# Kernel tuning notes

Measured on AMD Instinct MI355X. Metric: run time of the kernel, lower is better.

Reference implementation:

```python
import jax, jax.numpy as jnp
import numpy as np

DIM = 192
HEADS = 6
HEAD_DIM = DIM // HEADS  # 32
N = 64                   # prod(window_size) = 4*4*4
BW = 4096                # num_windows * B
NEG = -1e9               # finite stand-in for -inf additive mask


def setup_inputs() -> dict:
    key = jax.random.key(0)
    k_x, k_m, k_qkv, k_p, k_pb = jax.random.split(key, 5)
    x = jax.random.normal(k_x, (BW, N, N and 192))  # (BW, N, C)
    x = jax.random.normal(k_x, (BW, N, DIM), dtype=jnp.float32)
    # Shifted-window style additive mask: block-diagonal groups of tokens.
    # Each window gets a random group id per token; tokens attend only within
    # their group (0), cross-group gets NEG. Diagonal always allowed.
    gid = jax.random.randint(k_m, (BW, N), 0, 3)  # (BW, N) group ids in {0,1,2}
    same = gid[:, :, None] == gid[:, None, :]     # (BW, N, N) bool
    mask = jnp.where(same, 0.0, NEG).astype(jnp.float32)[:, None, :, :]  # (BW,1,N,N)
    w_qkv = jax.random.normal(k_qkv, (3 * DIM, DIM), dtype=jnp.float32) * (DIM ** -0.5)
    w_proj = jax.random.normal(k_p, (DIM, DIM), dtype=jnp.float32) * (DIM ** -0.5)
    b_proj = jax.random.normal(k_pb, (DIM,), dtype=jnp.float32) * 0.02
    return {"x": x, "mask": mask, "w_qkv": w_qkv, "w_proj": w_proj, "b_proj": b_proj}


def reference(x, mask, w_qkv, w_proj, b_proj):
    b, n, c = x.shape
    scale = HEAD_DIM ** -0.5
    # qkv linear (no bias) then split: 'b n (three heads c) -> three b heads n c'
    qkv = jnp.einsum('bnc,dc->bnd', x, w_qkv)               # (b, n, 3*C)
    qkv = qkv.reshape(b, n, 3, HEADS, HEAD_DIM)
    qkv = jnp.transpose(qkv, (2, 0, 3, 1, 4))               # (3, b, heads, n, hd)
    q, k, v = qkv[0], qkv[1], qkv[2]
    q = q * scale
    # scaled_dot_product_attention with additive mask (scale=1 since q pre-scaled)
    scores = jnp.einsum('bhqd,bhkd->bhqk', q, k) + mask     # (b, heads, n, n)
    probs = jax.nn.softmax(scores, axis=-1)
    out = jnp.einsum('bhqk,bhkd->bhqd', probs, v)           # (b, heads, n, hd)
    # 'b k n c -> b n (k c)'
    out = jnp.transpose(out, (0, 2, 1, 3)).reshape(b, n, c)
    # output projection (bias=True in nn.Linear default)
    return jnp.einsum('bnc,dc->bnd', out, w_proj) + b_proj
```

## Files before the change

kernel.cpp:

```cpp
#include <hip/hip_runtime.h>

#define NTOK 64
#define DIM 192
#define HD 32

#define RS  200
#define VTS 68
#define WQN (576 * DIM)
#define WPN (DIM * DIM)

typedef __attribute__((ext_vector_type(8))) short short8;
typedef __attribute__((ext_vector_type(4))) float floatx4;
typedef __attribute__((ext_vector_type(2))) unsigned int uint2v;

__device__ __forceinline__ short f2bf(float f) {
    union { float f; unsigned int u; } c; c.f = f;
    unsigned int r = (c.u + 0x7FFFu + ((c.u >> 16) & 1u)) >> 16;
    return (short)(unsigned short)r;
}

__device__ __forceinline__ unsigned pkbf(float a, float b) {
    unsigned ua = __float_as_uint(a); ua += 0x7FFFu + ((ua >> 16) & 1u);
    unsigned ub = __float_as_uint(b); ub += 0x7FFFu + ((ub >> 16) & 1u);
    return __builtin_amdgcn_perm(ub, ua, 0x07060302u);
}

__device__ __forceinline__ short8 cvt8(const float* p) {
    const float4* v = reinterpret_cast<const float4*>(p);
    float4 lo = v[0], hi = v[1];
    union { unsigned u[4]; short8 s; } r;
    r.u[0] = pkbf(lo.x, lo.y);
    r.u[1] = pkbf(lo.z, lo.w);
    r.u[2] = pkbf(hi.x, hi.y);
    r.u[3] = pkbf(hi.z, hi.w);
    return r.s;
}

__device__ __forceinline__ short8 qshuf(floatx4 v0, floatx4 v1, int lane) {
    const int q = lane >> 4;
    const unsigned p0a = pkbf(v0[0], v0[1]);
    const unsigned p0b = pkbf(v0[2], v0[3]);
    const unsigned p1a = pkbf(v1[0], v1[1]);
    const unsigned p1b = pkbf(v1[2], v1[3]);
    const int s0 = (lane & 15) | ((q & 1) << 5);
    const int s1 = s0 + 16;
    const unsigned l0 = (unsigned)__shfl((int)p0a, s0);
    const unsigned h0 = (unsigned)__shfl((int)p1a, s0);
    const unsigned l1 = (unsigned)__shfl((int)p0b, s0);
    const unsigned h1 = (unsigned)__shfl((int)p1b, s0);
    const unsigned l2 = (unsigned)__shfl((int)p0a, s1);
    const unsigned h2 = (unsigned)__shfl((int)p1a, s1);
    const unsigned l3 = (unsigned)__shfl((int)p0b, s1);
    const unsigned h3 = (unsigned)__shfl((int)p1b, s1);
    const bool hi = q >= 2;
    union { unsigned u[4]; short8 s; } ret;
    ret.u[0] = hi ? h0 : l0;
    ret.u[1] = hi ? h1 : l1;
    ret.u[2] = hi ? h2 : l2;
    ret.u[3] = hi ? h3 : l3;
    return ret.s;
}

__global__ void wprep(const float* __restrict__ wqkv, const float* __restrict__ wproj,
                      short* __restrict__ wqb, short* __restrict__ wpb) {
    const int i = blockIdx.x * 256 + (int)threadIdx.x;
    for (int e = i; e < WQN; e += 192 * 256) {
        float v = wqkv[e];
        if (e < DIM * DIM) v *= 0.17677669529663688f;
        wqb[e] = f2bf(v);
    }
    for (int e = i; e < WPN; e += 192 * 256) wpb[e] = f2bf(wproj[e]);
}

template <int WS>
__global__ __launch_bounds__(256, 2)
void wattn_fused(const float* __restrict__ x, const float* __restrict__ mask,
                 const float* __restrict__ wqkv, const float* __restrict__ wproj,
                 const float* __restrict__ bproj, float* __restrict__ out,
                 const short* __restrict__ wqb, const short* __restrict__ wpb) {
    __shared__ short ksm[NTOK * RS];
    __shared__ short vsT[DIM * VTS];
    __shared__ short osm[NTOK * RS];

    const int bw   = blockIdx.x;
    const int tid  = (int)threadIdx.x;
    const int wave = tid >> 6;
    const int lane = tid & 63;
    const int r    = lane & 15;
    const int q    = lane >> 4;

    const float* xb = x + (size_t)bw * (NTOK * DIM);

    auto ldq = [&](int off) -> short8 {
        if constexpr (WS) return *reinterpret_cast<const short8*>(wqb + off);
        else              return cvt8(wqkv + off);
    };
    auto ldp = [&](int off) -> short8 {
        if constexpr (WS) return *reinterpret_cast<const short8*>(wpb + off);
        else              return cvt8(wproj + off);
    };

    {
        short8 a[4][6];
        #pragma unroll
        for (int mt = 0; mt < 4; ++mt) {
            #pragma unroll
            for (int s = 0; s < 6; ++s)
                a[mt][s] = cvt8(xb + (mt * 16 + r) * DIM + s * 32 + q * 8);
        }

        if (wave < 2) {
            #pragma unroll 1
            for (int nt = 0; nt < 6; ++nt) {
                const int dk = wave * 96 + nt * 16;
                floatx4 acc[4];
                #pragma unroll
                for (int mt = 0; mt < 4; ++mt) acc[mt] = (floatx4){0.f, 0.f, 0.f, 0.f};
                #pragma unroll
                for (int s = 0; s < 6; ++s) {
                    const short8 b8 = ldq((DIM + dk + r) * DIM + s * 32 + q * 8);
                    #pragma unroll
                    for (int mt = 0; mt < 4; ++mt)
                        acc[mt] = __builtin_amdgcn_mfma_f32_16x16x32_bf16(b8, a[mt][s], acc[mt], 0, 0, 0);
                }
                #pragma unroll
                for (int mt = 0; mt < 4; ++mt) {
                    uint2v u;
                    u.x = pkbf(acc[mt][0], acc[mt][1]);
                    u.y = pkbf(acc[mt][2], acc[mt][3]);
                    *reinterpret_cast<uint2v*>(ksm + (mt * 16 + r) * RS + dk + q * 4) = u;
                }
            }
        } else {
            #pragma unroll 1
            for (int nt = 0; nt < 6; ++nt) {
                const int dv = (wave - 2) * 96 + nt * 16;
                floatx4 acc[4];
                #pragma unroll
                for (int mt = 0; mt < 4; ++mt) acc[mt] = (floatx4){0.f, 0.f, 0.f, 0.f};
                #pragma unroll
                for (int s = 0; s < 6; ++s) {
                    const short8 b8 = ldq((2 * DIM + dv + r) * DIM + s * 32 + q * 8);
                    #pragma unroll
                    for (int mt = 0; mt < 4; ++mt)
                        acc[mt] = __builtin_amdgcn_mfma_f32_16x16x32_bf16(a[mt][s], b8, acc[mt], 0, 0, 0);
                }
                #pragma unroll
                for (int mt = 0; mt < 4; ++mt) {
                    uint2v u;
                    u.x = pkbf(acc[mt][0], acc[mt][1]);
                    u.y = pkbf(acc[mt][2], acc[mt][3]);
                    *reinterpret_cast<uint2v*>(vsT + (dv + r) * VTS + mt * 16 + q * 4) = u;
                }
            }
        }
    }
    __builtin_amdgcn_sched_barrier(0);
    __syncthreads();

    const float* mb  = mask + (size_t)bw * (NTOK * NTOK);
    const float* mbl = mb + 256 * q + r;

    #pragma unroll 1
    for (int i = 0; i < 3; ++i) {
        const int uu = wave * 3 + i, h = uu >> 1, half = uu & 1;

        float mv[2][4][4];
        #pragma unroll
        for (int qt = 0; qt < 2; ++qt)
            #pragma unroll
            for (int kt = 0; kt < 4; ++kt)
                #pragma unroll
                for (int g = 0; g < 4; ++g)
                    mv[qt][kt][g] = mbl[kt * 1024 + g * 64 + half * 32 + qt * 16];

        floatx4 qa[2][2];
        #pragma unroll
        for (int dt = 0; dt < 2; ++dt)
            #pragma unroll
            for (int qt = 0; qt < 2; ++qt) qa[dt][qt] = (floatx4){0.f, 0.f, 0.f, 0.f};
        #pragma unroll
        for (int s = 0; s < 6; ++s) {
            const short8 w0 = ldq((h * HD + r) * DIM + s * 32 + q * 8);
            const short8 w1 = ldq((h * HD + 16 + r) * DIM + s * 32 + q * 8);
            #pragma unroll
            for (int qt = 0; qt < 2; ++qt) {
                const short8 xf = cvt8(xb + ((half * 2 + qt) * 16 + r) * DIM + s * 32 + q * 8);
                qa[0][qt] = __builtin_amdgcn_mfma_f32_16x16x32_bf16(w0, xf, qa[0][qt], 0, 0, 0);
                qa[1][qt] = __builtin_amdgcn_mfma_f32_16x16x32_bf16(w1, xf, qa[1][qt], 0, 0, 0);
            }
        }
        if constexpr (!WS) {
            #pragma unroll
            for (int dt = 0; dt < 2; ++dt)
                #pragma unroll
                for (int qt = 0; qt < 2; ++qt)
                    #pragma unroll
                    for (int g = 0; g < 4; ++g)
                        qa[dt][qt][g] *= 0.17677669529663688f;
        }
        short8 bq0 = qshuf(qa[0][0], qa[1][0], lane);
        short8 bq1 = qshuf(qa[0][1], qa[1][1], lane);

        short8 bk[4];
        #pragma unroll
        for (int kt = 0; kt < 4; ++kt)
            bk[kt] = *reinterpret_cast<const short8*>(ksm + (kt * 16 + r) * RS + h * HD + q * 8);

        floatx4 sa[4][2];
        #pragma unroll
        for (int kt = 0; kt < 4; ++kt) {
            floatx4 z = (floatx4){0.f, 0.f, 0.f, 0.f};
            sa[kt][0] = __builtin_amdgcn_mfma_f32_16x16x32_bf16(bk[kt], bq0, z, 0, 0, 0);
            sa[kt][1] = __builtin_amdgcn_mfma_f32_16x16x32_bf16(bk[kt], bq1, z, 0, 0, 0);
        }
        #pragma unroll
        for (int kt = 0; kt < 4; ++kt)
            #pragma unroll
            for (int qt = 0; qt < 2; ++qt)
                #pragma unroll
                for (int g = 0; g < 4; ++g)
                    sa[kt][qt][g] += mv[qt][kt][g];

        float rinv[2];
        #pragma unroll
        for (int qt = 0; qt < 2; ++qt) {
            float mx = sa[0][qt][0];
            #pragma unroll
            for (int kt = 0; kt < 4; ++kt)
                #pragma unroll
                for (int g = 0; g < 4; ++g) mx = fmaxf(mx, sa[kt][qt][g]);
            mx = fmaxf(mx, __shfl_xor(mx, 16));
            mx = fmaxf(mx, __shfl_xor(mx, 32));
            float sm = 0.f;
            #pragma unroll
            for (int kt = 0; kt < 4; ++kt) {
                #pragma unroll
                for (int g = 0; g < 4; ++g) {
                    float p = __expf(sa[kt][qt][g] - mx);
                    sa[kt][qt][g] = p;
                    sm += p;
                }
            }
            sm += __shfl_xor(sm, 16);
            sm += __shfl_xor(sm, 32);
            rinv[qt] = 1.0f / sm;
        }

        short8 ap[2][2];
        #pragma unroll
        for (int qt = 0; qt < 2; ++qt) {
            #pragma unroll
            for (int kk = 0; kk < 2; ++kk)
                ap[qt][kk] = qshuf(sa[2 * kk][qt], sa[2 * kk + 1][qt], lane);
        }

        short8 bv[2][2];
        #pragma unroll
        for (int nv = 0; nv < 2; ++nv)
            #pragma unroll
            for (int kk = 0; kk < 2; ++kk)
                bv[nv][kk] = *reinterpret_cast<const short8*>(
                    vsT + (h * HD + nv * 16 + r) * VTS + kk * 32 + q * 8);

        #pragma unroll
        for (int qt = 0; qt < 2; ++qt) {
            #pragma unroll
            for (int nv = 0; nv < 2; ++nv) {
                floatx4 o = (floatx4){0.f, 0.f, 0.f, 0.f};
                o = __builtin_amdgcn_mfma_f32_16x16x32_bf16(bv[nv][0], ap[qt][0], o, 0, 0, 0);
                o = __builtin_amdgcn_mfma_f32_16x16x32_bf16(bv[nv][1], ap[qt][1], o, 0, 0, 0);
                uint2v u;
                u.x = pkbf(o[0] * rinv[qt], o[1] * rinv[qt]);
                u.y = pkbf(o[2] * rinv[qt], o[3] * rinv[qt]);
                *reinterpret_cast<uint2v*>(
                    osm + (half * 32 + qt * 16 + r) * RS + h * HD + nv * 16 + q * 4) = u;
            }
        }
    }
    __syncthreads();

    short8 ao[4][6];
    #pragma unroll
    for (int mt = 0; mt < 4; ++mt) {
        #pragma unroll
        for (int s = 0; s < 6; ++s)
            ao[mt][s] = *reinterpret_cast<const short8*>(osm + (mt * 16 + r) * RS + s * 32 + q * 8);
    }

    float* ob = out + (size_t)bw * (NTOK * DIM);
    #pragma unroll 1
    for (int nt = 0; nt < 3; ++nt) {
        const int d0 = wave * 48 + nt * 16;
        const float4 b4 = *reinterpret_cast<const float4*>(bproj + d0 + q * 4);
        floatx4 acc[4];
        #pragma unroll
        for (int mt = 0; mt < 4; ++mt) acc[mt] = (floatx4){b4.x, b4.y, b4.z, b4.w};
        #pragma unroll
        for (int s = 0; s < 6; ++s) {
            const short8 w8 = ldp((d0 + r) * DIM + s * 32 + q * 8);
            #pragma unroll
            for (int mt = 0; mt < 4; ++mt)
                acc[mt] = __builtin_amdgcn_mfma_f32_16x16x32_bf16(w8, ao[mt][s], acc[mt], 0, 0, 0);
        }
        #pragma unroll
        for (int mt = 0; mt < 4; ++mt) {
            float4 st;
            st.x = acc[mt][0]; st.y = acc[mt][1]; st.z = acc[mt][2]; st.w = acc[mt][3];
            *reinterpret_cast<float4*>(ob + (mt * 16 + r) * DIM + d0 + q * 4) = st;
        }
    }
}

extern "C" void kernel_launch(void* const* d_in, const int* in_sizes, int n_in,
                              void* d_out, int out_size, void* d_ws, size_t ws_size,
                              hipStream_t stream) {
    const float* x    = (const float*)d_in[0];
    const float* mask = (const float*)d_in[1];
    const float* wqkv = (const float*)d_in[2];
    const float* wp   = (const float*)d_in[3];
    const float* bp   = (const float*)d_in[4];
    float* out = (float*)d_out;
    const int nblocks = in_sizes[0] / (NTOK * DIM);
    const size_t need = (size_t)(WQN + WPN) * sizeof(short);
    if (d_ws != nullptr && ws_size >= need) {
        short* wqb = (short*)d_ws;
        short* wpb = wqb + WQN;
        wprep<<<192, 256, 0, stream>>>(wqkv, wp, wqb, wpb);
        wattn_fused<1><<<nblocks, 256, 0, stream>>>(x, mask, wqkv, wp, bp, out, wqb, wpb);
    } else {
        wattn_fused<0><<<nblocks, 256, 0, stream>>>(x, mask, wqkv, wp, bp, out, nullptr, nullptr);
    }
}
```

Before: 700.7 us.

## Process eight windows per block with register-prefetched x and LDS-staged mask

Each block now loops over eight windows instead of one. The next window's x is prefetched into registers while the current one computes, and the mask is loaded coalesced and staged through shared memory instead of scattered per-lane loads. Q is computed from the already converted x registers rather than re-reading x from global memory. Launch bounds drop to one block per SM because of the larger register footprint and extra LDS, which lowers occupancy and cuts the grid to 512 blocks. Any window count not divisible by eight would be left unprocessed.

```diff
diff --git a/kernel.cpp b/kernel.cpp
--- a/kernel.cpp
+++ b/kernel.cpp
@@ -3,9 +3,11 @@
 #define NTOK 64
 #define DIM 192
 #define HD 32
+#define W 8
 
 #define RS  200
 #define VTS 68
+#define MS  68
 #define WQN (576 * DIM)
 #define WPN (DIM * DIM)
 
@@ -73,7 +75,7 @@
 }
 
 template <int WS>
-__global__ __launch_bounds__(256, 2)
+__global__ __launch_bounds__(256, 1)
 void wattn_fused(const float* __restrict__ x, const float* __restrict__ mask,
                  const float* __restrict__ wqkv, const float* __restrict__ wproj,
                  const float* __restrict__ bproj, float* __restrict__ out,
@@ -81,15 +83,14 @@
     __shared__ short ksm[NTOK * RS];
     __shared__ short vsT[DIM * VTS];
     __shared__ short osm[NTOK * RS];
-
-    const int bw   = blockIdx.x;
+    __shared__ float mlds[NTOK * MS];
+
+    const int bw0  = (int)blockIdx.x * W;
     const int tid  = (int)threadIdx.x;
     const int wave = tid >> 6;
     const int lane = tid & 63;
     const int r    = lane & 15;
     const int q    = lane >> 4;
-
-    const float* xb = x + (size_t)bw * (NTOK * DIM);
 
     auto ldq = [&](int off) -> short8 {
         if constexpr (WS) return *reinterpret_cast<const short8*>(wqb + off);
@@ -100,14 +101,46 @@
         else              return cvt8(wproj + off);
     };
 
-    {
+    float4 xp[4][6][2];
+    auto xload = [&](const float* xb) {
+        #pragma unroll
+        for (int mt = 0; mt < 4; ++mt) {
+            #pragma unroll
+            for (int s = 0; s < 6; ++s) {
+                const float4* v = reinterpret_cast<const float4*>(
+                    xb + (mt * 16 + r) * DIM + s * 32 + q * 8);
+                xp[mt][s][0] = v[0];
+                xp[mt][s][1] = v[1];
+            }
+        }
+    };
+    xload(x + (size_t)bw0 * (NTOK * DIM));
+
+    #pragma unroll 1
+    for (int w = 0; w < W; ++w) {
+        const int bw = bw0 + w;
+
         short8 a[4][6];
         #pragma unroll
         for (int mt = 0; mt < 4; ++mt) {
             #pragma unroll
-            for (int s = 0; s < 6; ++s)
-                a[mt][s] = cvt8(xb + (mt * 16 + r) * DIM + s * 32 + q * 8);
-        }
+            for (int s = 0; s < 6; ++s) {
+                union { unsigned u[4]; short8 s8; } t;
+                t.u[0] = pkbf(xp[mt][s][0].x, xp[mt][s][0].y);
+                t.u[1] = pkbf(xp[mt][s][0].z, xp[mt][s][0].w);
+                t.u[2] = pkbf(xp[mt][s][1].x, xp[mt][s][1].y);
+                t.u[3] = pkbf(xp[mt][s][1].z, xp[mt][s][1].w);
+                a[mt][s] = t.s8;
+            }
+        }
+
+        const float* mbW = mask + (size_t)bw * (NTOK * NTOK);
+        float4 mreg[4];
+        #pragma unroll
+        for (int it = 0; it < 4; ++it)
+            mreg[it] = *reinterpret_cast<const float4*>(mbW + it * 1024 + tid * 4);
+
+        if (w + 1 < W) xload(x + (size_t)(bw + 1) * (NTOK * DIM));
 
         if (wave < 2) {
             #pragma unroll 1
@@ -154,161 +187,151 @@
                 }
             }
         }
-    }
-    __builtin_amdgcn_sched_barrier(0);
-    __syncthreads();
-
-    const float* mb  = mask + (size_t)bw * (NTOK * NTOK);
-    const float* mbl = mb + 256 * q + r;
-
-    #pragma unroll 1
-    for (int i = 0; i < 3; ++i) {
-        const int uu = wave * 3 + i, h = uu >> 1, half = uu & 1;
-
-        float mv[2][4][4];
-        #pragma unroll
-        for (int qt = 0; qt < 2; ++qt)
+        #pragma unroll
+        for (int it = 0; it < 4; ++it)
+            *reinterpret_cast<float4*>(&mlds[(it * 16 + (tid >> 4)) * MS + (tid & 15) * 4]) = mreg[it];
+        __syncthreads();
+
+        #pragma unroll 1
+        for (int i = 0; i < 3; ++i) {
+            const int uu = wave * 3 + i, h = uu >> 1, half = uu & 1;
+
+            floatx4 qa[2][2];
+            #pragma unroll
+            for (int dt = 0; dt < 2; ++dt)
+                #pragma unroll
+                for (int qt = 0; qt < 2; ++qt) qa[dt][qt] = (floatx4){0.f, 0.f, 0.f, 0.f};
+            #pragma unroll
+            for (int s = 0; s < 6; ++s) {
+                const short8 w0 = ldq((h * HD + r) * DIM + s * 32 + q * 8);
+                const short8 w1 = ldq((h * HD + 16 + r) * DIM + s * 32 + q * 8);
+                #pragma unroll
+                for (int qt = 0; qt < 2; ++qt) {
+                    qa[0][qt] = __builtin_amdgcn_mfma_f32_16x16x32_bf16(w0, a[half * 2 + qt][s], qa[0][qt], 0, 0, 0);
+                    qa[1][qt] = __builtin_amdgcn_mfma_f32_16x16x32_bf16(w1, a[half * 2 + qt][s], qa[1][qt], 0, 0, 0);
+                }
+            }
+            if constexpr (!WS) {
+                #pragma unroll
+                for (int dt = 0; dt < 2; ++dt)
+                    #pragma unroll
+                    for (int qt = 0; qt < 2; ++qt)
+                        #pragma unroll
+                        for (int g = 0; g < 4; ++g)
+                            qa[dt][qt][g] *= 0.17677669529663688f;
+            }
+            short8 bq0 = qshuf(qa[0][0], qa[1][0], lane);
+            short8 bq1 = qshuf(qa[0][1], qa[1][1], lane);
+
+            short8 bk[4];
             #pragma unroll
             for (int kt = 0; kt < 4; ++kt)
-                #pragma unroll
-                for (int g = 0; g < 4; ++g)
-                    mv[qt][kt][g] = mbl[kt * 1024 + g * 64 + half * 32 + qt * 16];
-
-        floatx4 qa[2][2];
-        #pragma unroll
-        for (int dt = 0; dt < 2; ++dt)
-            #pragma unroll
-            for (int qt = 0; qt < 2; ++qt) qa[dt][qt] = (floatx4){0.f, 0.f, 0.f, 0.f};
-        #pragma unroll
-        for (int s = 0; s < 6; ++s) {
-            const short8 w0 = ldq((h * HD + r) * DIM + s * 32 + q * 8);
-            const short8 w1 = ldq((h * HD + 16 + r) * DIM + s * 32 + q * 8);
+                bk[kt] = *reinterpret_cast<const short8*>(ksm + (kt * 16 + r) * RS + h * HD + q * 8);
+
+            floatx4 sa[4][2];
+            #pragma unroll
+            for (int kt = 0; kt < 4; ++kt) {
+                floatx4 z = (floatx4){0.f, 0.f, 0.f, 0.f};
+                sa[kt][0] = __builtin_amdgcn_mfma_f32_16x16x32_bf16(bk[kt], bq0, z, 0, 0, 0);
+                sa[kt][1] = __builtin_amdgcn_mfma_f32_16x16x32_bf16(bk[kt], bq1, z, 0, 0, 0);
+            }
+            #pragma unroll
+            for (int kt = 0; kt < 4; ++kt)
+                #pragma unroll
+                for (int qt = 0; qt < 2; ++qt)
+                    #pragma unroll
+                    for (int g = 0; g < 4; ++g)
+                        sa[kt][qt][g] += mlds[(kt * 16 + 4 * q + g) * MS + half * 32 + qt * 16 + r];
+
+            float rinv[2];
             #pragma unroll
             for (int qt = 0; qt < 2; ++qt) {
-                const short8 xf = cvt8(xb + ((half * 2 + qt) * 16 + r) * DIM + s * 32 + q * 8);
-                qa[0][qt] = __builtin_amdgcn_mfma_f32_16x16x32_bf16(w0, xf, qa[0][qt], 0, 0, 0);
-                qa[1][qt] = __builtin_amdgcn_mfma_f32_16x16x32_bf16(w1, xf, qa[1][qt], 0, 0, 0);
-            }
-        }
-        if constexpr (!WS) {
-            #pragma unroll
-            for (int dt = 0; dt < 2; ++dt)
-                #pragma unroll
-                for (int qt = 0; qt < 2; ++qt)
-                    #pragma unroll
-                    for (int g = 0; g < 4; ++g)
-                        qa[dt][qt][g] *= 0.17677669529663688f;
-        }
-        short8 bq0 = qshuf(qa[0][0], qa[1][0], lane);
-        short8 bq1 = qshuf(qa[0][1], qa[1][1], lane);
-
-        short8 bk[4];
-        #pragma unroll
-        for (int kt = 0; kt < 4; ++kt)
-            bk[kt] = *reinterpret_cast<const short8*>(ksm + (kt * 16 + r) * RS + h * HD + q * 8);
-
-        floatx4 sa[4][2];
-        #pragma unroll
-        for (int kt = 0; kt < 4; ++kt) {
-            floatx4 z = (floatx4){0.f, 0.f, 0.f, 0.f};
-            sa[kt][0] = __builtin_amdgcn_mfma_f32_16x16x32_bf16(bk[kt], bq0, z, 0, 0, 0);
-            sa[kt][1] = __builtin_amdgcn_mfma_f32_16x16x32_bf16(bk[kt], bq1, z, 0, 0, 0);
-        }
-        #pragma unroll
-        for (int kt = 0; kt < 4; ++kt)
-            #pragma unroll
-            for (int qt = 0; qt < 2; ++qt)
-                #pragma unroll
-                for (int g = 0; g < 4; ++g)
-                    sa[kt][qt][g] += mv[qt][kt][g];
-
-        float rinv[2];
-        #pragma unroll
-        for (int qt = 0; qt < 2; ++qt) {
-            float mx = sa[0][qt][0];
-            #pragma unroll
-            for (int kt = 0; kt < 4; ++kt)
-                #pragma unroll
-                for (int g = 0; g < 4; ++g) mx = fmaxf(mx, sa[kt][qt][g]);
-            mx = fmaxf(mx, __shfl_xor(mx, 16));
-            mx = fmaxf(mx, __shfl_xor(mx, 32));
-            float sm = 0.f;
-            #pragma unroll
-            for (int kt = 0; kt < 4; ++kt) {
-                #pragma unroll
-                for (int g = 0; g < 4; ++g) {
-                    float p = __expf(sa[kt][qt][g] - mx);
-                    sa[kt][qt][g] = p;
-                    sm += p;
-                }
-            }
-            sm += __shfl_xor(sm, 16);
-            sm += __shfl_xor(sm, 32);
-            rinv[qt] = 1.0f / sm;
-        }
-
-        short8 ap[2][2];
-        #pragma unroll
-        for (int qt = 0; qt < 2; ++qt) {
-            #pragma unroll
-            for (int kk = 0; kk < 2; ++kk)
-                ap[qt][kk] = qshuf(sa[2 * kk][qt], sa[2 * kk + 1][qt], lane);
-        }
-
-        short8 bv[2][2];
-        #pragma unroll
-        for (int nv = 0; nv < 2; ++nv)
-            #pragma unroll
-            for (int kk = 0; kk < 2; ++kk)
-                bv[nv][kk] = *reinterpret_cast<const short8*>(
-                    vsT + (h * HD + nv * 16 + r) * VTS + kk * 32 + q * 8);
-
-        #pragma unroll
-        for (int qt = 0; qt < 2; ++qt) {
-            #pragma unroll
-            for (int nv = 0; nv < 2; ++nv) {
-                floatx4 o = (floatx4){0.f, 0.f, 0.f, 0.f};
-                o = __builtin_amdgcn_mfma_f32_16x16x32_bf16(bv[nv][0], ap[qt][0], o, 0, 0, 0);
-                o = __builtin_amdgcn_mfma_f32_16x16x32_bf16(bv[nv][1], ap[qt][1], o, 0, 0, 0);
-                uint2v u;
-                u.x = pkbf(o[0] * rinv[qt], o[1] * rinv[qt]);
-                u.y = pkbf(o[2] * rinv[qt], o[3] * rinv[qt]);
-                *reinterpret_cast<uint2v*>(
-                    osm + (half * 32 + qt * 16 + r) * RS + h * HD + nv * 16 + q * 4) = u;
-            }
-        }
-    }
-    __syncthreads();
-
-    short8 ao[4][6];
-    #pragma unroll
-    for (int mt = 0; mt < 4; ++mt) {
-        #pragma unroll
-        for (int s = 0; s < 6; ++s)
-            ao[mt][s] = *reinterpret_cast<const short8*>(osm + (mt * 16 + r) * RS + s * 32 + q * 8);
-    }
-
-    float* ob = out + (size_t)bw * (NTOK * DIM);
-    #pragma unroll 1
-    for (int nt = 0; nt < 3; ++nt) {
-        const int d0 = wave * 48 + nt * 16;
-        const float4 b4 = *reinterpret_cast<const float4*>(bproj + d0 + q * 4);
-        floatx4 acc[4];
-        #pragma unroll
-        for (int mt = 0; mt < 4; ++mt) acc[mt] = (floatx4){b4.x, b4.y, b4.z, b4.w};
-        #pragma unroll
-        for (int s = 0; s < 6; ++s) {
-            const short8 w8 = ldp((d0 + r) * DIM + s * 32 + q * 8);
-            #pragma unroll
-            for (int mt = 0; mt < 4; ++mt)
-                acc[mt] = __builtin_amdgcn_mfma_f32_16x16x32_bf16(w8, ao[mt][s], acc[mt], 0, 0, 0);
-        }
+                float mx = sa[0][qt][0];
+                #pragma unroll
+                for (int kt = 0; kt < 4; ++kt)
+                    #pragma unroll
+                    for (int g = 0; g < 4; ++g) mx = fmaxf(mx, sa[kt][qt][g]);
+                mx = fmaxf(mx, __shfl_xor(mx, 16));
+                mx = fmaxf(mx, __shfl_xor(mx, 32));
+                float sm = 0.f;
+                #pragma unroll
+                for (int kt = 0; kt < 4; ++kt) {
+                    #pragma unroll
+                    for (int g = 0; g < 4; ++g) {
+                        float p = __expf(sa[kt][qt][g] - mx);
+                        sa[kt][qt][g] = p;
+                        sm += p;
+                    }
+                }
+                sm += __shfl_xor(sm, 16);
+                sm += __shfl_xor(sm, 32);
+                rinv[qt] = 1.0f / sm;
+            }
+
+            short8 ap[2][2];
+            #pragma unroll
+            for (int qt = 0; qt < 2; ++qt) {
+                #pragma unroll
+                for (int kk = 0; kk < 2; ++kk)
+                    ap[qt][kk] = qshuf(sa[2 * kk][qt], sa[2 * kk + 1][qt], lane);
+            }
+
+            short8 bv[2][2];
+            #pragma unroll
+            for (int nv = 0; nv < 2; ++nv)
+                #pragma unroll
+                for (int kk = 0; kk < 2; ++kk)
+                    bv[nv][kk] = *reinterpret_cast<const short8*>(
+                        vsT + (h * HD + nv * 16 + r) * VTS + kk * 32 + q * 8);
+
+            #pragma unroll
+            for (int qt = 0; qt < 2; ++qt) {
+                #pragma unroll
+                for (int nv = 0; nv < 2; ++nv) {
+                    floatx4 o = (floatx4){0.f, 0.f, 0.f, 0.f};
+                    o = __builtin_amdgcn_mfma_f32_16x16x32_bf16(bv[nv][0], ap[qt][0], o, 0, 0, 0);
+                    o = __builtin_amdgcn_mfma_f32_16x16x32_bf16(bv[nv][1], ap[qt][1], o, 0, 0, 0);
+                    uint2v u;
+                    u.x = pkbf(o[0] * rinv[qt], o[1] * rinv[qt]);
+                    u.y = pkbf(o[2] * rinv[qt], o[3] * rinv[qt]);
+                    *reinterpret_cast<uint2v*>(
+                        osm + (half * 32 + qt * 16 + r) * RS + h * HD + nv * 16 + q * 4) = u;
+                }
+            }
+        }
+        __syncthreads();
+
+        short8 ao[4][6];
         #pragma unroll
         for (int mt = 0; mt < 4; ++mt) {
-            float4 st;
-            st.x = acc[mt][0]; st.y = acc[mt][1]; st.z = acc[mt][2]; st.w = acc[mt][3];
-            *reinterpret_cast<float4*>(ob + (mt * 16 + r) * DIM + d0 + q * 4) = st;
-        }
+            #pragma unroll
+            for (int s = 0; s < 6; ++s)
+                ao[mt][s] = *reinterpret_cast<const short8*>(osm + (mt * 16 + r) * RS + s * 32 + q * 8);
+        }
+
+        float* ob = out + (size_t)bw * (NTOK * DIM);
+        #pragma unroll 1
+        for (int nt = 0; nt < 3; ++nt) {
+            const int d0 = wave * 48 + nt * 16;
+            const float4 b4 = *reinterpret_cast<const float4*>(bproj + d0 + q * 4);
+            floatx4 acc[4];
+            #pragma unroll
+            for (int mt = 0; mt < 4; ++mt) acc[mt] = (floatx4){b4.x, b4.y, b4.z, b4.w};
+            #pragma unroll
+            for (int s = 0; s < 6; ++s) {
+                const short8 w8 = ldp((d0 + r) * DIM + s * 32 + q * 8);
+                #pragma unroll
+                for (int mt = 0; mt < 4; ++mt)
+                    acc[mt] = __builtin_amdgcn_mfma_f32_16x16x32_bf16(w8, ao[mt][s], acc[mt], 0, 0, 0);
+            }
+            #pragma unroll
+            for (int mt = 0; mt < 4; ++mt) {
+                float4 st;
+                st.x = acc[mt][0]; st.y = acc[mt][1]; st.z = acc[mt][2]; st.w = acc[mt][3];
+                *reinterpret_cast<float4*>(ob + (mt * 16 + r) * DIM + d0 + q * 4) = st;
+            }
+        }
+        __syncthreads();
     }
 }
 
@@ -321,7 +344,8 @@
     const float* wp   = (const float*)d_in[3];
     const float* bp   = (const float*)d_in[4];
     float* out = (float*)d_out;
-    const int nblocks = in_sizes[0] / (NTOK * DIM);
+    const int nwin = in_sizes[0] / (NTOK * DIM);
+    const int nblocks = nwin / W;
     const size_t need = (size_t)(WQN + WPN) * sizeof(short);
     if (d_ws != nullptr && ws_size >= need) {
         short* wqb = (short*)d_ws;
```

New measurement: 937.4 us. 33.8% more time.

## Split fused window attention into QKV projection and attention/output kernels

Applied to the files above, without the earlier changes.

Replaces the single fused kernel with two kernels. The first computes Q, K and V for each window using all four waves and writes them as bf16 in an LDS-ready padded layout to workspace. The second bulk-copies that blob into shared memory and runs attention plus the output projection. The aim is better load balance (previously waves were idle during part of the projection) and higher occupancy for the projection step. The cost is an extra global round-trip of about 80 KB per window and a second launch, and the path only runs when the workspace is large enough.

```diff
diff --git a/kernel.cpp b/kernel.cpp
--- a/kernel.cpp
+++ b/kernel.cpp
@@ -4,8 +4,11 @@
 #define DIM 192
 #define HD 32
 
-#define RS  200
-#define VTS 68
+#define RS   200
+#define VTS  68
+#define QBLK (NTOK * RS)
+#define VBLK (DIM * VTS)
+#define WBLOB (2 * QBLK + VBLK)
 #define WQN (576 * DIM)
 #define WPN (DIM * DIM)
 
@@ -72,6 +75,235 @@
     for (int e = i; e < WPN; e += 192 * 256) wpb[e] = f2bf(wproj[e]);
 }
 
+__global__ __launch_bounds__(256, 3)
+void qkv_proj(const float* __restrict__ x, const short* __restrict__ wqb,
+              short* __restrict__ qkv) {
+    const int bw   = blockIdx.x;
+    const int tid  = (int)threadIdx.x;
+    const int wave = tid >> 6;
+    const int lane = tid & 63;
+    const int r    = lane & 15;
+    const int q    = lane >> 4;
+
+    const float* xb = x + (size_t)bw * (NTOK * DIM);
+    short* qb = qkv + (size_t)bw * WBLOB;
+    short* kb = qb + QBLK;
+    short* vb = kb + QBLK;
+
+    short8 a[4][6];
+    #pragma unroll
+    for (int mt = 0; mt < 4; ++mt) {
+        #pragma unroll
+        for (int s = 0; s < 6; ++s)
+            a[mt][s] = cvt8(xb + (mt * 16 + r) * DIM + s * 32 + q * 8);
+    }
+
+    #pragma unroll 1
+    for (int nt = 0; nt < 9; ++nt) {
+        const int d0 = wave * 144 + nt * 16;
+        floatx4 acc[4];
+        #pragma unroll
+        for (int mt = 0; mt < 4; ++mt) acc[mt] = (floatx4){0.f, 0.f, 0.f, 0.f};
+        if (d0 < 2 * DIM) {
+            #pragma unroll
+            for (int s = 0; s < 6; ++s) {
+                const short8 b8 = *reinterpret_cast<const short8*>(
+                    wqb + (d0 + r) * DIM + s * 32 + q * 8);
+                #pragma unroll
+                for (int mt = 0; mt < 4; ++mt)
+                    acc[mt] = __builtin_amdgcn_mfma_f32_16x16x32_bf16(b8, a[mt][s], acc[mt], 0, 0, 0);
+            }
+            short* dst = (d0 < DIM) ? qb : kb;
+            const int dc = (d0 < DIM) ? d0 : d0 - DIM;
+            #pragma unroll
+            for (int mt = 0; mt < 4; ++mt) {
+                uint2v u;
+                u.x = pkbf(acc[mt][0], acc[mt][1]);
+                u.y = pkbf(acc[mt][2], acc[mt][3]);
+                *reinterpret_cast<uint2v*>(dst + (mt * 16 + r) * RS + dc + q * 4) = u;
+            }
+        } else {
+            const int dv = d0 - 2 * DIM;
+            #pragma unroll
+            for (int s = 0; s < 6; ++s) {
+                const short8 b8 = *reinterpret_cast<const short8*>(
+                    wqb + (d0 + r) * DIM + s * 32 + q * 8);
+                #pragma unroll
+                for (int mt = 0; mt < 4; ++mt)
+                    acc[mt] = __builtin_amdgcn_mfma_f32_16x16x32_bf16(a[mt][s], b8, acc[mt], 0, 0, 0);
+            }
+            #pragma unroll
+            for (int mt = 0; mt < 4; ++mt) {
+                uint2v u;
+                u.x = pkbf(acc[mt][0], acc[mt][1]);
+                u.y = pkbf(acc[mt][2], acc[mt][3]);
+                *reinterpret_cast<uint2v*>(vb + (dv + r) * VTS + mt * 16 + q * 4) = u;
+            }
+        }
+    }
+}
+
+__global__ __launch_bounds__(256, 2)
+void attn_out(const short* __restrict__ qkv, const float* __restrict__ mask,
+              const short* __restrict__ wpb, const float* __restrict__ bproj,
+              float* __restrict__ out) {
+    __shared__ short blob[38912];
+
+    const int bw   = blockIdx.x;
+    const int tid  = (int)threadIdx.x;
+    const int wave = tid >> 6;
+    const int lane = tid & 63;
+    const int r    = lane & 15;
+    const int q    = lane >> 4;
+
+    const short* src = qkv + (size_t)bw * WBLOB;
+    #pragma unroll
+    for (int j = 0; j < 19; ++j) {
+        const int o = (tid + 256 * j) * 8;
+        *reinterpret_cast<short8*>(blob + o) = *reinterpret_cast<const short8*>(src + o);
+    }
+    __syncthreads();
+
+    short* ksm = blob + QBLK;
+    short* vsT = blob + 2 * QBLK;
+
+    short8 bq[3][2];
+    #pragma unroll
+    for (int i = 0; i < 3; ++i) {
+        const int uu = wave * 3 + i, h = uu >> 1, half = uu & 1;
+        #pragma unroll
+        for (int qt = 0; qt < 2; ++qt)
+            bq[i][qt] = *reinterpret_cast<const short8*>(
+                blob + (half * 32 + qt * 16 + r) * RS + h * HD + q * 8);
+    }
+    __syncthreads();
+    short* osm = blob;
+
+    const float* mbl = mask + (size_t)bw * (NTOK * NTOK) + 256 * q + r;
+
+    #pragma unroll
+    for (int i = 0; i < 3; ++i) {
+        const int uu = wave * 3 + i, h = uu >> 1, half = uu & 1;
+
+        float mv[2][4][4];
+        #pragma unroll
+        for (int qt = 0; qt < 2; ++qt)
+            #pragma unroll
+            for (int kt = 0; kt < 4; ++kt)
+                #pragma unroll
+                for (int g = 0; g < 4; ++g)
+                    mv[qt][kt][g] = mbl[kt * 1024 + g * 64 + half * 32 + qt * 16];
+
+        short8 bk[4];
+        #pragma unroll
+        for (int kt = 0; kt < 4; ++kt)
+            bk[kt] = *reinterpret_cast<const short8*>(ksm + (kt * 16 + r) * RS + h * HD + q * 8);
+
+        floatx4 sa[4][2];
+        #pragma unroll
+        for (int kt = 0; kt < 4; ++kt) {
+            floatx4 z = (floatx4){0.f, 0.f, 0.f, 0.f};
+            sa[kt][0] = __builtin_amdgcn_mfma_f32_16x16x32_bf16(bk[kt], bq[i][0], z, 0, 0, 0);
+            sa[kt][1] = __builtin_amdgcn_mfma_f32_16x16x32_bf16(bk[kt], bq[i][1], z, 0, 0, 0);
+        }
+        #pragma unroll
+        for (int kt = 0; kt < 4; ++kt)
+            #pragma unroll
+            for (int qt = 0; qt < 2; ++qt)
+                #pragma unroll
+                for (int g = 0; g < 4; ++g)
+                    sa[kt][qt][g] += mv[qt][kt][g];
+
+        float rinv[2];
+        #pragma unroll
+        for (int qt = 0; qt < 2; ++qt) {
+            float mx = sa[0][qt][0];
+            #pragma unroll
+            for (int kt = 0; kt < 4; ++kt)
+                #pragma unroll
+                for (int g = 0; g < 4; ++g) mx = fmaxf(mx, sa[kt][qt][g]);
+            mx = fmaxf(mx, __shfl_xor(mx, 16));
+            mx = fmaxf(mx, __shfl_xor(mx, 32));
+            float sm = 0.f;
+            #pragma unroll
+            for (int kt = 0; kt < 4; ++kt) {
+                #pragma unroll
+                for (int g = 0; g < 4; ++g) {
+                    float p = __expf(sa[kt][qt][g] - mx);
+                    sa[kt][qt][g] = p;
+                    sm += p;
+                }
+            }
+            sm += __shfl_xor(sm, 16);
+            sm += __shfl_xor(sm, 32);
+            rinv[qt] = 1.0f / sm;
+        }
+
+        short8 ap[2][2];
+        #pragma unroll
+        for (int qt = 0; qt < 2; ++qt) {
+            #pragma unroll
+            for (int kk = 0; kk < 2; ++kk)
+                ap[qt][kk] = qshuf(sa[2 * kk][qt], sa[2 * kk + 1][qt], lane);
+        }
+
+        short8 bv[2][2];
+        #pragma unroll
+        for (int nv = 0; nv < 2; ++nv)
+            #pragma unroll
+            for (int kk = 0; kk < 2; ++kk)
+                bv[nv][kk] = *reinterpret_cast<const short8*>(
+                    vsT + (h * HD + nv * 16 + r) * VTS + kk * 32 + q * 8);
+
+        #pragma unroll
+        for (int qt = 0; qt < 2; ++qt) {
+            #pragma unroll
+            for (int nv = 0; nv < 2; ++nv) {
+                floatx4 o = (floatx4){0.f, 0.f, 0.f, 0.f};
+                o = __builtin_amdgcn_mfma_f32_16x16x32_bf16(bv[nv][0], ap[qt][0], o, 0, 0, 0);
+                o = __builtin_amdgcn_mfma_f32_16x16x32_bf16(bv[nv][1], ap[qt][1], o, 0, 0, 0);
+                uint2v u;
+                u.x = pkbf(o[0] * rinv[qt], o[1] * rinv[qt]);
+                u.y = pkbf(o[2] * rinv[qt], o[3] * rinv[qt]);
+                *reinterpret_cast<uint2v*>(
+                    osm + (half * 32 + qt * 16 + r) * RS + h * HD + nv * 16 + q * 4) = u;
+            }
+        }
+    }
+    __syncthreads();
+
+    short8 ao[4][6];
+    #pragma unroll
+    for (int mt = 0; mt < 4; ++mt) {
+        #pragma unroll
+        for (int s = 0; s < 6; ++s)
+            ao[mt][s] = *reinterpret_cast<const short8*>(osm + (mt * 16 + r) * RS + s * 32 + q * 8);
+    }
+
+    float* ob = out + (size_t)bw * (NTOK * DIM);
+    #pragma unroll
+    for (int nt = 0; nt < 3; ++nt) {
+        const int d0 = wave * 48 + nt * 16;
+        const float4 b4 = *reinterpret_cast<const float4*>(bproj + d0 + q * 4);
+        floatx4 acc[4];
+        #pragma unroll
+        for (int mt = 0; mt < 4; ++mt) acc[mt] = (floatx4){b4.x, b4.y, b4.z, b4.w};
+        #pragma unroll
+        for (int s = 0; s < 6; ++s) {
+            const short8 w8 = *reinterpret_cast<const short8*>(wpb + (d0 + r) * DIM + s * 32 + q * 8);
+            #pragma unroll
+            for (int mt = 0; mt < 4; ++mt)
+                acc[mt] = __builtin_amdgcn_mfma_f32_16x16x32_bf16(w8, ao[mt][s], acc[mt], 0, 0, 0);
+        }
+        #pragma unroll
+        for (int mt = 0; mt < 4; ++mt) {
+            float4 st;
+            st.x = acc[mt][0]; st.y = acc[mt][1]; st.z = acc[mt][2]; st.w = acc[mt][3];
+            *reinterpret_cast<float4*>(ob + (mt * 16 + r) * DIM + d0 + q * 4) = st;
+        }
+    }
+}
+
 template <int WS>
 __global__ __launch_bounds__(256, 2)
 void wattn_fused(const float* __restrict__ x, const float* __restrict__ mask,
@@ -108,7 +340,6 @@
             for (int s = 0; s < 6; ++s)
                 a[mt][s] = cvt8(xb + (mt * 16 + r) * DIM + s * 32 + q * 8);
         }
-
         if (wave < 2) {
             #pragma unroll 1
             for (int nt = 0; nt < 6; ++nt) {
@@ -158,13 +389,11 @@
     __builtin_amdgcn_sched_barrier(0);
     __syncthreads();
 
-    const float* mb  = mask + (size_t)bw * (NTOK * NTOK);
-    const float* mbl = mb + 256 * q + r;
+    const float* mbl = mask + (size_t)bw * (NTOK * NTOK) + 256 * q + r;
 
     #pragma unroll 1
     for (int i = 0; i < 3; ++i) {
         const int uu = wave * 3 + i, h = uu >> 1, half = uu & 1;
-
         float mv[2][4][4];
         #pragma unroll
         for (int qt = 0; qt < 2; ++qt)
@@ -321,14 +550,24 @@
     const float* wp   = (const float*)d_in[3];
     const float* bp   = (const float*)d_in[4];
     float* out = (float*)d_out;
-    const int nblocks = in_sizes[0] / (NTOK * DIM);
-    const size_t need = (size_t)(WQN + WPN) * sizeof(short);
-    if (d_ws != nullptr && ws_size >= need) {
+    const int nwin = in_sizes[0] / (NTOK * DIM);
+
+    const size_t needw     = (size_t)(WQN + WPN) * sizeof(short);
+    const size_t needsplit = needw + ((size_t)nwin * WBLOB + 256) * sizeof(short);
+
+    if (d_ws != nullptr && ws_size >= needsplit) {
+        short* wqb  = (short*)d_ws;
+        short* wpb  = wqb + WQN;
+        short* qkvb = wpb + WPN;
+        wprep<<<192, 256, 0, stream>>>(wqkv, wp, wqb, wpb);
+        qkv_proj<<<nwin, 256, 0, stream>>>(x, wqb, qkvb);
+        attn_out<<<nwin, 256, 0, stream>>>(qkvb, mask, wpb, bp, out);
+    } else if (d_ws != nullptr && ws_size >= needw) {
         short* wqb = (short*)d_ws;
         short* wpb = wqb + WQN;
         wprep<<<192, 256, 0, stream>>>(wqkv, wp, wqb, wpb);
-        wattn_fused<1><<<nblocks, 256, 0, stream>>>(x, mask, wqkv, wp, bp, out, wqb, wpb);
+        wattn_fused<1><<<nwin, 256, 0, stream>>>(x, mask, wqkv, wp, bp, out, wqb, wpb);
     } else {
-        wattn_fused<0><<<nblocks, 256, 0, stream>>>(x, mask, wqkv, wp, bp, out, nullptr, nullptr);
-    }
-}
+        wattn_fused<0><<<nwin, 256, 0, stream>>>(x, mask, wqkv, wp, bp, out, nullptr, nullptr);
+    }
+}
```

Measured after the change: 713.5 us. No clear change (+1.8%).

## Hoist mask loads and Q projection ahead of the K/V barrier

Applied to the files above, without the earlier changes.

Splits the per-wave attention loop into phases. All mask values for the wave's three head-halves are loaded up front, and the Q projection for all three units is computed before the __syncthreads that waits for K/V to be written to shared memory. The goal is to overlap global mask-load latency and Q-projection MFMA work with the barrier wait. In exchange, register pressure rises sharply: 96 mask floats plus six short8 Q fragments are now held live, which may reduce occupancy or cause spills.

```diff
diff --git a/kernel.cpp b/kernel.cpp
--- a/kernel.cpp
+++ b/kernel.cpp
@@ -156,24 +156,26 @@
         }
     }
     __builtin_amdgcn_sched_barrier(0);
-    __syncthreads();
-
-    const float* mb  = mask + (size_t)bw * (NTOK * NTOK);
-    const float* mbl = mb + 256 * q + r;
-
-    #pragma unroll 1
-    for (int i = 0; i < 3; ++i) {
-        const int uu = wave * 3 + i, h = uu >> 1, half = uu & 1;
-
-        float mv[2][4][4];
+
+    const float* mbl = mask + (size_t)bw * (NTOK * NTOK) + 256 * q + r;
+    float mv[3][2][4][4];
+    #pragma unroll
+    for (int u = 0; u < 3; ++u) {
+        const int half = (wave * 3 + u) & 1;
         #pragma unroll
         for (int qt = 0; qt < 2; ++qt)
             #pragma unroll
             for (int kt = 0; kt < 4; ++kt)
                 #pragma unroll
                 for (int g = 0; g < 4; ++g)
-                    mv[qt][kt][g] = mbl[kt * 1024 + g * 64 + half * 32 + qt * 16];
-
+                    mv[u][qt][kt][g] = mbl[kt * 1024 + g * 64 + half * 32 + qt * 16];
+    }
+    __builtin_amdgcn_sched_barrier(0);
+
+    short8 bq[3][2];
+    #pragma unroll
+    for (int u = 0; u < 3; ++u) {
+        const int uu = wave * 3 + u, h = uu >> 1, half = uu & 1;
         floatx4 qa[2][2];
         #pragma unroll
         for (int dt = 0; dt < 2; ++dt)
@@ -199,8 +201,14 @@
                     for (int g = 0; g < 4; ++g)
                         qa[dt][qt][g] *= 0.17677669529663688f;
         }
-        short8 bq0 = qshuf(qa[0][0], qa[1][0], lane);
-        short8 bq1 = qshuf(qa[0][1], qa[1][1], lane);
+        bq[u][0] = qshuf(qa[0][0], qa[1][0], lane);
+        bq[u][1] = qshuf(qa[0][1], qa[1][1], lane);
+    }
+    __syncthreads();
+
+    #pragma unroll
+    for (int u = 0; u < 3; ++u) {
+        const int uu = wave * 3 + u, h = uu >> 1, half = uu & 1;
 
         short8 bk[4];
         #pragma unroll
@@ -211,8 +219,8 @@
         #pragma unroll
         for (int kt = 0; kt < 4; ++kt) {
             floatx4 z = (floatx4){0.f, 0.f, 0.f, 0.f};
-            sa[kt][0] = __builtin_amdgcn_mfma_f32_16x16x32_bf16(bk[kt], bq0, z, 0, 0, 0);
-            sa[kt][1] = __builtin_amdgcn_mfma_f32_16x16x32_bf16(bk[kt], bq1, z, 0, 0, 0);
+            sa[kt][0] = __builtin_amdgcn_mfma_f32_16x16x32_bf16(bk[kt], bq[u][0], z, 0, 0, 0);
+            sa[kt][1] = __builtin_amdgcn_mfma_f32_16x16x32_bf16(bk[kt], bq[u][1], z, 0, 0, 0);
         }
         #pragma unroll
         for (int kt = 0; kt < 4; ++kt)
@@ -220,7 +228,7 @@
             for (int qt = 0; qt < 2; ++qt)
                 #pragma unroll
                 for (int g = 0; g < 4; ++g)
-                    sa[kt][qt][g] += mv[qt][kt][g];
+                    sa[kt][qt][g] += mv[u][qt][kt][g];
 
         float rinv[2];
         #pragma unroll
@@ -270,11 +278,11 @@
                 floatx4 o = (floatx4){0.f, 0.f, 0.f, 0.f};
                 o = __builtin_amdgcn_mfma_f32_16x16x32_bf16(bv[nv][0], ap[qt][0], o, 0, 0, 0);
                 o = __builtin_amdgcn_mfma_f32_16x16x32_bf16(bv[nv][1], ap[qt][1], o, 0, 0, 0);
-                uint2v u;
-                u.x = pkbf(o[0] * rinv[qt], o[1] * rinv[qt]);
-                u.y = pkbf(o[2] * rinv[qt], o[3] * rinv[qt]);
+                uint2v uo;
+                uo.x = pkbf(o[0] * rinv[qt], o[1] * rinv[qt]);
+                uo.y = pkbf(o[2] * rinv[qt], o[3] * rinv[qt]);
                 *reinterpret_cast<uint2v*>(
-                    osm + (half * 32 + qt * 16 + r) * RS + h * HD + nv * 16 + q * 4) = u;
+                    osm + (half * 32 + qt * 16 + r) * RS + h * HD + nv * 16 + q * 4) = uo;
             }
         }
     }
@@ -321,14 +329,14 @@
     const float* wp   = (const float*)d_in[3];
     const float* bp   = (const float*)d_in[4];
     float* out = (float*)d_out;
-    const int nblocks = in_sizes[0] / (NTOK * DIM);
-    const size_t need = (size_t)(WQN + WPN) * sizeof(short);
-    if (d_ws != nullptr && ws_size >= need) {
+    const int nwin = in_sizes[0] / (NTOK * DIM);
+    const size_t needw = (size_t)(WQN + WPN) * sizeof(short);
+    if (d_ws != nullptr && ws_size >= needw) {
         short* wqb = (short*)d_ws;
         short* wpb = wqb + WQN;
         wprep<<<192, 256, 0, stream>>>(wqkv, wp, wqb, wpb);
-        wattn_fused<1><<<nblocks, 256, 0, stream>>>(x, mask, wqkv, wp, bp, out, wqb, wpb);
+        wattn_fused<1><<<nwin, 256, 0, stream>>>(x, mask, wqkv, wp, bp, out, wqb, wpb);
     } else {
-        wattn_fused<0><<<nblocks, 256, 0, stream>>>(x, mask, wqkv, wp, bp, out, nullptr, nullptr);
-    }
-}
+        wattn_fused<0><<<nwin, 256, 0, stream>>>(x, mask, wqkv, wp, bp, out, nullptr, nullptr);
+    }
+}
```

Result: faster. 681.8 us (-2.7%).
